# Performance work log

Measured on AMD Instinct MI355X. Metric: run time of the kernel, lower is better.

Reference implementation:

```python
import jax, jax.numpy as jnp
import numpy as np

DIM_M = 4
DIM_C = 4   # context dim
DIM_F = 4   # feature dim
DIM_Q = DIM_F + 1  # [scale | features]
B = 2_000_000


def setup_inputs() -> dict:
    key = jax.random.key(0)
    k1, k2, k3, k4 = jax.random.split(key, 4)
    xss = jax.random.normal(k1, (B, DIM_M, DIM_Q), dtype=jnp.float32)
    # ragged lengths in [1, DIM_M]
    seq_lengths = jax.random.randint(k2, (B,), 1, DIM_M + 1, dtype=jnp.int64)
    # torch.nn.Linear default init ~ U(-1/sqrt(fan_in), 1/sqrt(fan_in)); any small init is fine for a reference
    W_cob = jax.random.normal(k3, (DIM_C, DIM_F), dtype=jnp.float32) / np.sqrt(DIM_F).astype(np.float32)
    W_reg = jax.random.normal(k4, (DIM_M, DIM_C), dtype=jnp.float32) / np.sqrt(DIM_C).astype(np.float32)
    return {"xss": xss, "seq_lengths": seq_lengths, "W_cob": W_cob, "W_reg": W_reg}


def reference(xss, seq_lengths, W_cob, W_reg):
    # xss: [B, S, Q] with S = DIM_M, Q = DIM_F + 1
    scales = xss[..., 0:1]            # [B, S, 1]
    fs = xss[..., 1:]                 # [B, S, F]
    bs = jnp.einsum('bsf,cf->bsc', fs, W_cob)          # change_of_basis (no bias)
    valid = jnp.arange(DIM_M)[None, :] < seq_lengths[:, None]   # [B, S] ragged mask
    cs = bs * scales * valid[..., None].astype(bs.dtype)        # base_coordinates, masked
    context = cs.sum(axis=1)                                    # pool over valid prefix -> [B, C]
    ys = jnp.einsum('bc,mc->bm', context, W_reg)
    projs = jnp.einsum('bsm,bm->bs', bs, ys)                    # per-position dot with broadcast ys
    # ragged concat: only valid positions, in batch-major order (matches torch.cat of per-batch slices)
    return projs[valid][:, None]                                # [sum(seq_lengths), 1]
```

## Files before the change

### kernel.cpp

```cpp
#include <hip/hip_runtime.h>

#define NT 256
#define EPT 4
#define BLK_ELEMS (NT * EPT)

__global__ __launch_bounds__(NT) void tile_sum_kernel(const int* __restrict__ seq,
                                                      unsigned* __restrict__ blockTotal,
                                                      int n) {
    __shared__ unsigned wsum[4];
    const int tid = threadIdx.x, lane = tid & 63, wave = tid >> 6;
    const int base = blockIdx.x * BLK_ELEMS + tid * EPT;
    unsigned v = 0;
    if (base + EPT <= n) {
        int4 q = *(const int4*)(seq + base);
        v = (unsigned)(q.x + q.y + q.z + q.w);
    } else {
        for (int e = 0; e < EPT; e++)
            if (base + e < n) v += (unsigned)seq[base + e];
    }
    #pragma unroll
    for (int off = 32; off > 0; off >>= 1) v += __shfl_down(v, off);
    if (lane == 0) wsum[wave] = v;
    __syncthreads();
    if (tid == 0) blockTotal[blockIdx.x] = wsum[0] + wsum[1] + wsum[2] + wsum[3];
}

__global__ __launch_bounds__(NT) void main_kernel(const float* __restrict__ xss,
                                                  const int* __restrict__ seq,
                                                  const float* __restrict__ Wcob,
                                                  const float* __restrict__ Wreg,
                                                  const unsigned* __restrict__ blockTotal,
                                                  float* __restrict__ out,
                                                  int n) {
    __shared__ unsigned wred[4];
    __shared__ unsigned wtot[4];
    const int tid = threadIdx.x, lane = tid & 63, wave = tid >> 6;
    const int bid = blockIdx.x;
    const int base = bid * BLK_ELEMS + tid * EPT;

    int l[EPT];
    if (base + EPT <= n) {
        int4 q = *(const int4*)(seq + base);
        l[0] = q.x; l[1] = q.y; l[2] = q.z; l[3] = q.w;
    } else {
        #pragma unroll
        for (int e = 0; e < EPT; e++) l[e] = (base + e < n) ? seq[base + e] : 0;
    }
    const unsigned tsum = (unsigned)(l[0] + l[1] + l[2] + l[3]);

    unsigned acc = 0;
    for (int i = tid; i < bid; i += NT) acc += blockTotal[i];
    unsigned r = acc;
    #pragma unroll
    for (int off = 32; off > 0; off >>= 1) r += __shfl_down(r, off);
    if (lane == 0) wred[wave] = r;

    unsigned v = tsum;
    #pragma unroll
    for (int off = 1; off < 64; off <<= 1) {
        unsigned t = __shfl_up(v, off);
        if (lane >= off) v += t;
    }
    if (lane == 63) wtot[wave] = v;
    __syncthreads();
    const unsigned prefix = wred[0] + wred[1] + wred[2] + wred[3];
    unsigned woff = 0;
    #pragma unroll
    for (int w = 0; w < 4; w++) woff += (w < wave) ? wtot[w] : 0u;
    unsigned o = prefix + woff + (v - tsum);

    float wc[16], wr[16];
    #pragma unroll
    for (int i = 0; i < 16; i++) { wc[i] = Wcob[i]; wr[i] = Wreg[i]; }

    #pragma unroll
    for (int e = 0; e < EPT; e++) {
        const int gid = base + e;
        const int L = l[e];
        if (gid < n && L > 0) {
            const float* p = xss + (size_t)gid * 20;
            float4 v0 = *(const float4*)(p + 0);
            float4 v1 = *(const float4*)(p + 4);
            float4 v2 = *(const float4*)(p + 8);
            float4 v3 = *(const float4*)(p + 12);
            float4 v4 = *(const float4*)(p + 16);
            float x[20];
            x[0]=v0.x;  x[1]=v0.y;  x[2]=v0.z;  x[3]=v0.w;
            x[4]=v1.x;  x[5]=v1.y;  x[6]=v1.z;  x[7]=v1.w;
            x[8]=v2.x;  x[9]=v2.y;  x[10]=v2.z; x[11]=v2.w;
            x[12]=v3.x; x[13]=v3.y; x[14]=v3.z; x[15]=v3.w;
            x[16]=v4.x; x[17]=v4.y; x[18]=v4.z; x[19]=v4.w;

            float bs[4][4];
            #pragma unroll
            for (int s = 0; s < 4; s++) {
                #pragma unroll
                for (int c = 0; c < 4; c++) {
                    float a = 0.f;
                    #pragma unroll
                    for (int f = 0; f < 4; f++) a += x[s * 5 + 1 + f] * wc[c * 4 + f];
                    bs[s][c] = a;
                }
            }
            float ctx[4] = {0.f, 0.f, 0.f, 0.f};
            #pragma unroll
            for (int s = 0; s < 4; s++) {
                float m = (s < L) ? x[s * 5] : 0.f;
                #pragma unroll
                for (int c = 0; c < 4; c++) ctx[c] += bs[s][c] * m;
            }
            float ys[4];
            #pragma unroll
            for (int m = 0; m < 4; m++) {
                float a = 0.f;
                #pragma unroll
                for (int c = 0; c < 4; c++) a += ctx[c] * wr[m * 4 + c];
                ys[m] = a;
            }
            #pragma unroll
            for (int s = 0; s < 4; s++) {
                if (s < L) {
                    float a = 0.f;
                    #pragma unroll
                    for (int m = 0; m < 4; m++) a += bs[s][m] * ys[m];
                    out[o + s] = a;
                }
            }
            o += (unsigned)L;
        }
    }
}

extern "C" void kernel_launch(void* const* d_in, const int* in_sizes, int n_in,
                              void* d_out, int out_size, void* d_ws, size_t ws_size,
                              hipStream_t stream) {
    const float* xss  = (const float*)d_in[0];
    const int*   seq  = (const int*)d_in[1];
    const float* Wcob = (const float*)d_in[2];
    const float* Wreg = (const float*)d_in[3];
    float* out = (float*)d_out;

    int n  = in_sizes[1];
    int nb = (n + BLK_ELEMS - 1) / BLK_ELEMS;

    unsigned* blockTotal = (unsigned*)d_ws;

    tile_sum_kernel<<<nb, NT, 0, stream>>>(seq, blockTotal, n);
    main_kernel<<<nb, NT, 0, stream>>>(xss, seq, Wcob, Wreg, blockTotal, out, n);
}
```

Measured before the change: 271.4 us.

## Stage ragged outputs in LDS for coalesced stores and prefetch inputs early

New measurement: 241.9 us. 1.12x faster.

```diff
diff --git a/kernel.cpp b/kernel.cpp
--- a/kernel.cpp
+++ b/kernel.cpp
@@ -34,6 +34,8 @@
                                                   int n) {
     __shared__ unsigned wred[4];
     __shared__ unsigned wtot[4];
+    __shared__ float outbuf[BLK_ELEMS * 4];
+
     const int tid = threadIdx.x, lane = tid & 63, wave = tid >> 6;
     const int bid = blockIdx.x;
     const int base = bid * BLK_ELEMS + tid * EPT;
@@ -47,6 +49,12 @@
         for (int e = 0; e < EPT; e++) l[e] = (base + e < n) ? seq[base + e] : 0;
     }
     const unsigned tsum = (unsigned)(l[0] + l[1] + l[2] + l[3]);
+
+    const int cbase = (base + EPT <= n) ? base : (n - EPT);
+    const float4* px = (const float4*)(xss + (size_t)cbase * 20);
+    float4 q[20];
+    #pragma unroll
+    for (int i = 0; i < 20; i++) q[i] = px[i];
 
     unsigned acc = 0;
     for (int i = tid; i < bid; i += NT) acc += blockTotal[i];
@@ -64,71 +72,64 @@
     if (lane == 63) wtot[wave] = v;
     __syncthreads();
     const unsigned prefix = wred[0] + wred[1] + wred[2] + wred[3];
+    const unsigned total  = wtot[0] + wtot[1] + wtot[2] + wtot[3];
     unsigned woff = 0;
     #pragma unroll
     for (int w = 0; w < 4; w++) woff += (w < wave) ? wtot[w] : 0u;
-    unsigned o = prefix + woff + (v - tsum);
+    unsigned lo = woff + (v - tsum);
 
     float wc[16], wr[16];
     #pragma unroll
     for (int i = 0; i < 16; i++) { wc[i] = Wcob[i]; wr[i] = Wreg[i]; }
 
+    const float* x = (const float*)q;
+
     #pragma unroll
     for (int e = 0; e < EPT; e++) {
-        const int gid = base + e;
         const int L = l[e];
-        if (gid < n && L > 0) {
-            const float* p = xss + (size_t)gid * 20;
-            float4 v0 = *(const float4*)(p + 0);
-            float4 v1 = *(const float4*)(p + 4);
-            float4 v2 = *(const float4*)(p + 8);
-            float4 v3 = *(const float4*)(p + 12);
-            float4 v4 = *(const float4*)(p + 16);
-            float x[20];
-            x[0]=v0.x;  x[1]=v0.y;  x[2]=v0.z;  x[3]=v0.w;
-            x[4]=v1.x;  x[5]=v1.y;  x[6]=v1.z;  x[7]=v1.w;
-            x[8]=v2.x;  x[9]=v2.y;  x[10]=v2.z; x[11]=v2.w;
-            x[12]=v3.x; x[13]=v3.y; x[14]=v3.z; x[15]=v3.w;
-            x[16]=v4.x; x[17]=v4.y; x[18]=v4.z; x[19]=v4.w;
+        const float* xe = x + e * 20;
 
-            float bs[4][4];
+        float bs[4][4];
+        #pragma unroll
+        for (int s = 0; s < 4; s++) {
             #pragma unroll
-            for (int s = 0; s < 4; s++) {
-                #pragma unroll
-                for (int c = 0; c < 4; c++) {
-                    float a = 0.f;
-                    #pragma unroll
-                    for (int f = 0; f < 4; f++) a += x[s * 5 + 1 + f] * wc[c * 4 + f];
-                    bs[s][c] = a;
-                }
-            }
-            float ctx[4] = {0.f, 0.f, 0.f, 0.f};
-            #pragma unroll
-            for (int s = 0; s < 4; s++) {
-                float m = (s < L) ? x[s * 5] : 0.f;
-                #pragma unroll
-                for (int c = 0; c < 4; c++) ctx[c] += bs[s][c] * m;
-            }
-            float ys[4];
-            #pragma unroll
-            for (int m = 0; m < 4; m++) {
+            for (int c = 0; c < 4; c++) {
                 float a = 0.f;
                 #pragma unroll
-                for (int c = 0; c < 4; c++) a += ctx[c] * wr[m * 4 + c];
-                ys[m] = a;
+                for (int f = 0; f < 4; f++) a += xe[s * 5 + 1 + f] * wc[c * 4 + f];
+                bs[s][c] = a;
             }
+        }
+        float ctx[4] = {0.f, 0.f, 0.f, 0.f};
+        #pragma unroll
+        for (int s = 0; s < 4; s++) {
+            float m = (s < L) ? xe[s * 5] : 0.f;
             #pragma unroll
-            for (int s = 0; s < 4; s++) {
-                if (s < L) {
-                    float a = 0.f;
-                    #pragma unroll
-                    for (int m = 0; m < 4; m++) a += bs[s][m] * ys[m];
-                    out[o + s] = a;
-                }
+            for (int c = 0; c < 4; c++) ctx[c] += bs[s][c] * m;
+        }
+        float ys[4];
+        #pragma unroll
+        for (int m = 0; m < 4; m++) {
+            float a = 0.f;
+            #pragma unroll
+            for (int c = 0; c < 4; c++) a += ctx[c] * wr[m * 4 + c];
+            ys[m] = a;
+        }
+        #pragma unroll
+        for (int s = 0; s < 4; s++) {
+            if (s < L) {
+                float a = 0.f;
+                #pragma unroll
+                for (int m = 0; m < 4; m++) a += bs[s][m] * ys[m];
+                outbuf[lo + s] = a;
             }
-            o += (unsigned)L;
         }
+        lo += (unsigned)((L > 0) ? L : 0);
     }
+
+    __syncthreads();
+    for (unsigned i = tid; i < total; i += NT)
+        out[prefix + i] = outbuf[i];
 }
 
 extern "C" void kernel_launch(void* const* d_in, const int* in_sizes, int n_in,
```

## Stage input and output through LDS for coalesced loads and stores

Applied to the files above, without the earlier changes.

New measurement: 244.9 us. 1.11x faster.

```diff
diff --git a/kernel.cpp b/kernel.cpp
--- a/kernel.cpp
+++ b/kernel.cpp
@@ -3,6 +3,9 @@
 #define NT 256
 #define EPT 4
 #define BLK_ELEMS (NT * EPT)
+#define PASS_ELEMS 256
+#define NPASS (BLK_ELEMS / PASS_ELEMS)
+#define ELEM_B 80
 
 __global__ __launch_bounds__(NT) void tile_sum_kernel(const int* __restrict__ seq,
                                                       unsigned* __restrict__ blockTotal,
@@ -32,8 +35,12 @@
                                                   const unsigned* __restrict__ blockTotal,
                                                   float* __restrict__ out,
                                                   int n) {
+    __shared__ float4   inbuf[PASS_ELEMS * 5];
+    __shared__ unsigned offs[BLK_ELEMS + 1];
+    __shared__ float    outbuf[PASS_ELEMS * 4];
     __shared__ unsigned wred[4];
     __shared__ unsigned wtot[4];
+
     const int tid = threadIdx.x, lane = tid & 63, wave = tid >> 6;
     const int bid = blockIdx.x;
     const int base = bid * BLK_ELEMS + tid * EPT;
@@ -47,6 +54,17 @@
         for (int e = 0; e < EPT; e++) l[e] = (base + e < n) ? seq[base + e] : 0;
     }
     const unsigned tsum = (unsigned)(l[0] + l[1] + l[2] + l[3]);
+
+    const char* xb = (const char*)xss;
+    const size_t blk_byte = (size_t)bid * BLK_ELEMS * ELEM_B;
+    const size_t limit = (size_t)n * ELEM_B - 16;
+    auto stage_addr = [&](int p, int j) -> const float4* {
+        size_t a = blk_byte + (size_t)p * (PASS_ELEMS * ELEM_B) + (size_t)(j * NT + tid) * 16;
+        if (a > limit) a = limit;
+        return (const float4*)(xb + a);
+    };
+    float4 r0 = *stage_addr(0, 0), r1 = *stage_addr(0, 1), r2 = *stage_addr(0, 2),
+           r3 = *stage_addr(0, 3), r4 = *stage_addr(0, 4);
 
     unsigned acc = 0;
     for (int i = tid; i < bid; i += NT) acc += blockTotal[i];
@@ -67,67 +85,90 @@
     unsigned woff = 0;
     #pragma unroll
     for (int w = 0; w < 4; w++) woff += (w < wave) ? wtot[w] : 0u;
-    unsigned o = prefix + woff + (v - tsum);
+
+    unsigned run = woff + (v - tsum);
+    #pragma unroll
+    for (int e = 0; e < EPT; e++) {
+        offs[tid * EPT + e] = (run << 3) | (unsigned)l[e];
+        run += (unsigned)l[e];
+    }
+    if (tid == NT - 1) offs[BLK_ELEMS] = run << 3;
 
     float wc[16], wr[16];
     #pragma unroll
     for (int i = 0; i < 16; i++) { wc[i] = Wcob[i]; wr[i] = Wreg[i]; }
 
-    #pragma unroll
-    for (int e = 0; e < EPT; e++) {
-        const int gid = base + e;
-        const int L = l[e];
-        if (gid < n && L > 0) {
-            const float* p = xss + (size_t)gid * 20;
-            float4 v0 = *(const float4*)(p + 0);
-            float4 v1 = *(const float4*)(p + 4);
-            float4 v2 = *(const float4*)(p + 8);
-            float4 v3 = *(const float4*)(p + 12);
-            float4 v4 = *(const float4*)(p + 16);
-            float x[20];
-            x[0]=v0.x;  x[1]=v0.y;  x[2]=v0.z;  x[3]=v0.w;
-            x[4]=v1.x;  x[5]=v1.y;  x[6]=v1.z;  x[7]=v1.w;
-            x[8]=v2.x;  x[9]=v2.y;  x[10]=v2.z; x[11]=v2.w;
-            x[12]=v3.x; x[13]=v3.y; x[14]=v3.z; x[15]=v3.w;
-            x[16]=v4.x; x[17]=v4.y; x[18]=v4.z; x[19]=v4.w;
+    for (int p = 0; p < NPASS; ++p) {
+        __syncthreads();
+        inbuf[0 * NT + tid] = r0;
+        inbuf[1 * NT + tid] = r1;
+        inbuf[2 * NT + tid] = r2;
+        inbuf[3 * NT + tid] = r3;
+        inbuf[4 * NT + tid] = r4;
+        if (p + 1 < NPASS) {
+            r0 = *stage_addr(p + 1, 0);
+            r1 = *stage_addr(p + 1, 1);
+            r2 = *stage_addr(p + 1, 2);
+            r3 = *stage_addr(p + 1, 3);
+            r4 = *stage_addr(p + 1, 4);
+        }
+        __syncthreads();
 
-            float bs[4][4];
+        const unsigned pk = offs[p * PASS_ELEMS + tid];
+        const unsigned pb = offs[p * PASS_ELEMS] >> 3;
+        const unsigned pe = offs[(p + 1) * PASS_ELEMS] >> 3;
+        const int L = (int)(pk & 7u);
+        const unsigned oo = (pk >> 3) - pb;
+
+        const float4* ep = inbuf + tid * 5;
+        float4 A = ep[0], Bq = ep[1], C = ep[2], D = ep[3], E = ep[4];
+        float x[20];
+        x[0]=A.x;  x[1]=A.y;  x[2]=A.z;  x[3]=A.w;
+        x[4]=Bq.x; x[5]=Bq.y; x[6]=Bq.z; x[7]=Bq.w;
+        x[8]=C.x;  x[9]=C.y;  x[10]=C.z; x[11]=C.w;
+        x[12]=D.x; x[13]=D.y; x[14]=D.z; x[15]=D.w;
+        x[16]=E.x; x[17]=E.y; x[18]=E.z; x[19]=E.w;
+
+        float bs[4][4];
+        #pragma unroll
+        for (int s = 0; s < 4; s++) {
             #pragma unroll
-            for (int s = 0; s < 4; s++) {
-                #pragma unroll
-                for (int c = 0; c < 4; c++) {
-                    float a = 0.f;
-                    #pragma unroll
-                    for (int f = 0; f < 4; f++) a += x[s * 5 + 1 + f] * wc[c * 4 + f];
-                    bs[s][c] = a;
-                }
-            }
-            float ctx[4] = {0.f, 0.f, 0.f, 0.f};
-            #pragma unroll
-            for (int s = 0; s < 4; s++) {
-                float m = (s < L) ? x[s * 5] : 0.f;
-                #pragma unroll
-                for (int c = 0; c < 4; c++) ctx[c] += bs[s][c] * m;
-            }
-            float ys[4];
-            #pragma unroll
-            for (int m = 0; m < 4; m++) {
+            for (int c = 0; c < 4; c++) {
                 float a = 0.f;
                 #pragma unroll
-                for (int c = 0; c < 4; c++) a += ctx[c] * wr[m * 4 + c];
-                ys[m] = a;
+                for (int f = 0; f < 4; f++) a += x[s * 5 + 1 + f] * wc[c * 4 + f];
+                bs[s][c] = a;
             }
+        }
+        float ctx[4] = {0.f, 0.f, 0.f, 0.f};
+        #pragma unroll
+        for (int s = 0; s < 4; s++) {
+            float m = (s < L) ? x[s * 5] : 0.f;
             #pragma unroll
-            for (int s = 0; s < 4; s++) {
-                if (s < L) {
-                    float a = 0.f;
-                    #pragma unroll
-                    for (int m = 0; m < 4; m++) a += bs[s][m] * ys[m];
-                    out[o + s] = a;
-                }
+            for (int c = 0; c < 4; c++) ctx[c] += bs[s][c] * m;
+        }
+        float ys[4];
+        #pragma unroll
+        for (int m = 0; m < 4; m++) {
+            float a = 0.f;
+            #pragma unroll
+            for (int c = 0; c < 4; c++) a += ctx[c] * wr[m * 4 + c];
+            ys[m] = a;
+        }
+        #pragma unroll
+        for (int s = 0; s < 4; s++) {
+            if (s < L) {
+                float a = 0.f;
+                #pragma unroll
+                for (int m = 0; m < 4; m++) a += bs[s][m] * ys[m];
+                outbuf[oo + s] = a;
             }
-            o += (unsigned)L;
         }
+
+        __syncthreads();
+        const unsigned tp = pe - pb;
+        for (unsigned i = tid; i < tp; i += NT)
+            out[prefix + pb + i] = outbuf[i];
     }
 }
 
```
